# Performance work log

Measured on AMD Instinct MI355X. Metric: run time of the kernel, lower is better.

## Reference

```python
import jax, jax.numpy as jnp
import numpy as np

N_NODES = 100000
N_EDGES = 640000
D_IN = 128
D_OUT = 128
BN_EPS = 1e-5


def setup_inputs() -> dict:
    key = jax.random.key(0)
    k1, k2, k3, k4 = jax.random.split(key, 4)
    x = jax.random.normal(k1, (N_NODES, D_IN), dtype=jnp.float32)
    edge_index = jax.random.randint(k2, (2, N_EDGES), 0, N_NODES, dtype=jnp.int64)
    W = jax.random.normal(k3, (D_IN, D_OUT), dtype=jnp.float32) * (1.0 / np.sqrt(D_IN))
    b = jnp.zeros((D_OUT,), dtype=jnp.float32)
    gamma = jnp.ones((D_OUT,), dtype=jnp.float32)
    beta = jnp.zeros((D_OUT,), dtype=jnp.float32)
    return {"x": x, "edge_index": edge_index, "W": W, "b": b, "gamma": gamma, "beta": beta}


def reference(x, edge_index, W, b, gamma, beta):
    N = x.shape[0]
    # --- GCNConv: add self-loops, symmetric normalization ---
    loop = jnp.arange(N, dtype=edge_index.dtype)
    src = jnp.concatenate([edge_index[0], loop])  # [E+N]
    dst = jnp.concatenate([edge_index[1], loop])  # [E+N]
    deg = jax.ops.segment_sum(jnp.ones_like(dst, dtype=x.dtype), dst, num_segments=N)
    dinv = jax.lax.rsqrt(deg)  # deg >= 1 due to self-loops
    norm = dinv[src] * dinv[dst]  # [E+N]
    # linear transform first (PyG order), then gather-normalize-scatter
    h = x @ W  # [N, D_OUT]
    msg = h[src] * norm[:, None]  # [E+N, D_OUT]
    agg = jax.ops.segment_sum(msg, dst, num_segments=N) + b  # [N, D_OUT]
    # --- ReLU ---
    r = jax.nn.relu(agg)
    # --- BatchNorm over node axis (training-mode batch statistics) ---
    mean = r.mean(axis=0)
    var = r.var(axis=0)
    out = gamma * (r - mean) * jax.lax.rsqrt(var + BN_EPS) + beta
    # dropout: identity in eval/deterministic mode
    return out
```

## Files before the change

### kernel.cpp

```cpp
#include <hip/hip_runtime.h>
#include <hip/hip_bf16.h>

#define N_NODES 100000
#define N_EDGES 640000
#define D 128
#define BN_EPS 1e-5f
#define NB_FILL 2500
#define NB_CVT 6250
#define NREP 64
#define BM 64
#define CS_LD 130
#define SLOTS 16
#define OSLOTS 32

typedef __attribute__((ext_vector_type(8))) short short8;
typedef __attribute__((ext_vector_type(4))) float f32x4;

__device__ inline unsigned int f2bf(float f) {
    unsigned int u = __builtin_bit_cast(unsigned int, f);
    return (u + 0x7FFFu + ((u >> 16) & 1u)) >> 16;
}
__device__ inline float bflo(unsigned int p) { return __builtin_bit_cast(float, p << 16); }
__device__ inline float bfhi(unsigned int p) { return __builtin_bit_cast(float, p & 0xFFFF0000u); }

__global__ void k_zero(int* __restrict__ cnt, float* __restrict__ rep) {
    int i = blockIdx.x * 256 + threadIdx.x;
    if (i < N_NODES) cnt[i] = 0;
    if (i < NREP * 256) rep[i] = 0.0f;
}

__global__ __launch_bounds__(256) void k_prep(const int* __restrict__ ei, int* __restrict__ cnt,
                                              int* __restrict__ buck, int* __restrict__ buck2,
                                              const float* __restrict__ x, uint4* __restrict__ xb,
                                              const float* __restrict__ W,
                                              unsigned short* __restrict__ Wfrag) {
    const int bid = blockIdx.x;
    const int t = threadIdx.x;
    if (bid < NB_CVT) {
        int src = 0, d = 0;
        const bool has_e = (bid < NB_FILL);
        if (has_e) {
            const int e = bid * 256 + t;
            src = ei[e];
            d = ei[N_EDGES + e];
        }
        const size_t i = (size_t)bid * 256 + t;
        const float4* xg = (const float4*)x;
        float4 a = xg[2 * i], c = xg[2 * i + 1];
        int slot = -1;
        if (has_e) slot = atomicAdd(&cnt[d], 1);
        uint4 o;
        o.x = f2bf(a.x) | (f2bf(a.y) << 16);
        o.y = f2bf(a.z) | (f2bf(a.w) << 16);
        o.z = f2bf(c.x) | (f2bf(c.y) << 16);
        o.w = f2bf(c.z) | (f2bf(c.w) << 16);
        xb[i] = o;
        if (has_e) {
            if (slot < SLOTS) buck[(size_t)d * SLOTS + slot] = src;
            else if (slot < SLOTS + OSLOTS) buck2[(size_t)d * OSLOTS + slot - SLOTS] = src;
        }
    } else {
        const int i = (bid - NB_CVT) * 256 + t;
        const int e  = i & 7;
        const int l  = (i >> 3) & 63;
        const int ct = (i >> 9) & 7;
        const int kk = i >> 12;
        const int lr = l & 15, lk = l >> 4;
        const int k   = kk * 32 + lk * 8 + e;
        const int col = ct * 16 + lr;
        Wfrag[i] = (unsigned short)f2bf(W[(size_t)k * D + col]);
    }
}

__global__ __launch_bounds__(1024) void k_gmm(const int* __restrict__ buck,
                                              const int* __restrict__ buck2,
                                              const int* __restrict__ cnt,
                                              const unsigned int* __restrict__ xb,
                                              const unsigned short* __restrict__ Wfrag,
                                              const float* __restrict__ b,
                                              unsigned int* __restrict__ outb,
                                              float* __restrict__ rep) {
    __shared__ __align__(16) char U[BM * CS_LD * 4];
    unsigned int* As_u = (unsigned int*)U;
    float* Cs = (float*)U;
    __shared__ float lsum[16][32];
    __shared__ float lsq[16][32];

    const int t = threadIdx.x;
    const int w = t >> 6;
    const int l = t & 63;
    const int lr = l & 15;
    const int lk = l >> 4;
    const int r0 = blockIdx.x * BM;

    for (int rr = 0; rr < 4; ++rr) {
        const int lrow = w * 4 + rr;
        int n = r0 + lrow; if (n >= N_NODES) n = N_NODES - 1;
        const int deg = cnt[n];
        const float di = rsqrtf((float)(deg + 1));
        const unsigned int hv = xb[(size_t)n * 64 + l];
        const float dd = di * di;
        float ax = bflo(hv) * dd;
        float ay = bfhi(hv) * dd;

        const int m = (deg > SLOTS + OSLOTS) ? (SLOTS + OSLOTS) : deg;
        int s_l = 0; float f_l = 0.0f;
        if (l < m) {
            s_l = (l < SLOTS) ? buck[(size_t)n * SLOTS + l]
                              : buck2[(size_t)n * OSLOTS + l - SLOTS];
            f_l = rsqrtf((float)(cnt[s_l] + 1)) * di;
        }
        for (int k = 0; k < m; k += 8) {
            unsigned int v[8];
            float f[8];
#pragma unroll
            for (int i = 0; i < 8; ++i) {
                const int sj = __builtin_amdgcn_readlane(s_l, k + i);
                f[i] = __builtin_bit_cast(float,
                    __builtin_amdgcn_readlane(__builtin_bit_cast(int, f_l), k + i));
                v[i] = xb[(size_t)sj * 64 + l];
            }
#pragma unroll
            for (int i = 0; i < 8; ++i) {
                ax = fmaf(bflo(v[i]), f[i], ax);
                ay = fmaf(bfhi(v[i]), f[i], ay);
            }
        }
        As_u[lrow * 64 + ((((l >> 2) ^ (lrow & 15)) << 2) | (l & 3))] =
            f2bf(ax) | (f2bf(ay) << 16);
    }
    __syncthreads();

    const int arow = (w & 3) * 16 + lr;
    const uint4* As4 = (const uint4*)U;
    short8 a[4];
#pragma unroll
    for (int kk = 0; kk < 4; ++kk)
        a[kk] = *(const short8*)&As4[arow * 16 + ((kk * 4 + lk) ^ (arow & 15))];
    __syncthreads();

    const int ct0 = (w >> 2) * 2;
    f32x4 acc[2];
    acc[0] = (f32x4)(0.0f);
    acc[1] = (f32x4)(0.0f);
#pragma unroll
    for (int kk = 0; kk < 4; ++kk) {
#pragma unroll
        for (int c = 0; c < 2; ++c) {
            const short8 bb = *(const short8*)(Wfrag + ((((kk * 8 + ct0 + c) << 6) + l) << 3));
            acc[c] = __builtin_amdgcn_mfma_f32_16x16x32_bf16(a[kk], bb, acc[c], 0, 0, 0);
        }
    }

    float s[2] = {0.0f, 0.0f}, s2[2] = {0.0f, 0.0f};
#pragma unroll
    for (int c = 0; c < 2; ++c) {
        const int ct = ct0 + c;
        const float bias = b[ct * 16 + lr];
#pragma unroll
        for (int r = 0; r < 4; ++r) {
            const int lrow = (w & 3) * 16 + lk * 4 + r;
            const float v = fmaxf(acc[c][r] + bias, 0.0f);
            if (r0 + lrow < N_NODES) {
                s[c] += v;
                s2[c] = fmaf(v, v, s2[c]);
            }
            Cs[lrow * CS_LD + ct * 16 + lr] = v;
        }
    }
#pragma unroll
    for (int c = 0; c < 2; ++c) {
        s[c]  += __shfl_xor(s[c], 16);  s[c]  += __shfl_xor(s[c], 32);
        s2[c] += __shfl_xor(s2[c], 16); s2[c] += __shfl_xor(s2[c], 32);
    }
    if (l < 16) {
#pragma unroll
        for (int c = 0; c < 2; ++c) {
            lsum[w][c * 16 + lr] = s[c];
            lsq[w][c * 16 + lr]  = s2[c];
        }
    }
    __syncthreads();

#pragma unroll
    for (int i = 0; i < 1; ++i) { }
#pragma unroll
    for (int i = 0; i < 1; ++i) {
        const int v0 = t;
#pragma unroll
        for (int p = 0; p < 1; ++p) { }
    }
    {
        const int v = t;
        const int row = v >> 4;
        const int q   = v & 15;
        if (r0 + row < N_NODES) {
            const float* p = &Cs[row * CS_LD + q * 8];
            uint4 o;
            o.x = f2bf(p[0]) | (f2bf(p[1]) << 16);
            o.y = f2bf(p[2]) | (f2bf(p[3]) << 16);
            o.z = f2bf(p[4]) | (f2bf(p[5]) << 16);
            o.w = f2bf(p[6]) | (f2bf(p[7]) << 16);
            ((uint4*)outb)[(size_t)(r0 + row) * 16 + q] = o;
        }
    }

    if (t < 128) {
        const int g = t >> 5;
        const int cc = t & 31;
        const float ssum = lsum[4 * g + 0][cc] + lsum[4 * g + 1][cc]
                         + lsum[4 * g + 2][cc] + lsum[4 * g + 3][cc];
        const float ssq  = lsq[4 * g + 0][cc] + lsq[4 * g + 1][cc]
                         + lsq[4 * g + 2][cc] + lsq[4 * g + 3][cc];
        const int col = g * 32 + cc;
        float* r = rep + (blockIdx.x & (NREP - 1)) * 256;
        atomicAdd(&r[col],       ssum);
        atomicAdd(&r[128 + col], ssq);
    }
}

__global__ __launch_bounds__(256) void k_red(const float* __restrict__ rep,
                                             const float* __restrict__ gamma,
                                             const float* __restrict__ beta,
                                             float* __restrict__ sclsft) {
    __shared__ float sh[256];
    const int t = threadIdx.x;
    float s = 0.0f;
    for (int r = 0; r < NREP; ++r) s += rep[r * 256 + t];
    sh[t] = s;
    __syncthreads();
    if (t < 128) {
        const float inv_n = 1.0f / (float)N_NODES;
        const float mean = sh[t] * inv_n;
        const float var = sh[128 + t] * inv_n - mean * mean;
        const float sc = gamma[t] * rsqrtf(var + BN_EPS);
        sclsft[t]       = sc;
        sclsft[128 + t] = beta[t] - mean * sc;
    }
}

__global__ __launch_bounds__(256) void k_norm(const uint4* __restrict__ outb,
                                              float4* __restrict__ out,
                                              const float* __restrict__ sclsft) {
    __shared__ float sc[256];
    const int t = threadIdx.x;
    sc[t] = sclsft[t];
    __syncthreads();
    const int i = blockIdx.x * 256 + t;
    if (i >= N_NODES * 16) return;
    const int c0 = (i & 15) * 8;
    const uint4 v = outb[i];
    float4 o0, o1;
    o0.x = fmaf(bflo(v.x), sc[c0 + 0], sc[128 + c0 + 0]);
    o0.y = fmaf(bfhi(v.x), sc[c0 + 1], sc[128 + c0 + 1]);
    o0.z = fmaf(bflo(v.y), sc[c0 + 2], sc[128 + c0 + 2]);
    o0.w = fmaf(bfhi(v.y), sc[c0 + 3], sc[128 + c0 + 3]);
    o1.x = fmaf(bflo(v.z), sc[c0 + 4], sc[128 + c0 + 4]);
    o1.y = fmaf(bfhi(v.z), sc[c0 + 5], sc[128 + c0 + 5]);
    o1.z = fmaf(bflo(v.w), sc[c0 + 6], sc[128 + c0 + 6]);
    o1.w = fmaf(bfhi(v.w), sc[c0 + 7], sc[128 + c0 + 7]);
    out[(size_t)i * 2]     = o0;
    out[(size_t)i * 2 + 1] = o1;
}

extern "C" void kernel_launch(void* const* d_in, const int* in_sizes, int n_in,
                              void* d_out, int out_size, void* d_ws, size_t ws_size,
                              hipStream_t stream) {
    const float* x     = (const float*)d_in[0];
    const int*   ei    = (const int*)d_in[1];
    const float* W     = (const float*)d_in[2];
    const float* b     = (const float*)d_in[3];
    const float* gamma = (const float*)d_in[4];
    const float* beta  = (const float*)d_in[5];
    float* out = (float*)d_out;

    char* ws = (char*)d_ws;
    int*            cnt    = (int*)(ws + 0);
    float*          rep    = (float*)(ws + (512u << 10));
    float*          sclsft = (float*)(ws + (640u << 10));
    unsigned short* Wfrag  = (unsigned short*)(ws + (704u << 10));
    int*            buck   = (int*)(ws + (1024u << 10));
    int*            buck2  = (int*)(ws + (8192u << 10));
    unsigned int*   xb     = (unsigned int*)(ws + (24576u << 10));
    unsigned int*   outb   = (unsigned int*)(ws + (57344u << 10));

    k_zero<<<(N_NODES + 255) / 256, 256, 0, stream>>>(cnt, rep);
    k_prep<<<NB_CVT + 64, 256, 0, stream>>>(ei, cnt, buck, buck2, x, (uint4*)xb, W, Wfrag);
    k_gmm<<<(N_NODES + BM - 1) / BM, 1024, 0, stream>>>(buck, buck2, cnt, xb, Wfrag, b,
                                                        outb, rep);
    k_red<<<1, 256, 0, stream>>>(rep, gamma, beta, sclsft);
    k_norm<<<(N_NODES * 16 + 255) / 256, 256, 0, stream>>>((const uint4*)outb, (float4*)out,
                                                           sclsft);
}
```

Measured before the change: 120.0 us.

## Partition edge bucketing per XCD to cut cross-die atomic contention

Edge bucketing moves into 313 dedicated blocks, each handling 8 edges per thread. Counters and 8-slot buckets are replicated per XCD (indexed by blockIdx&7), so the atomics stay local to one die, and a shared overflow list catches the rest. A new k_dinv kernel sums the per-XCD counts into dinv and a packed prefix word that k_gmm uses to locate neighbour indices. k_zero is replaced by hipMemsetAsync. The change adds a launch, more metadata traffic, a scattered 8x bucket layout and prefix decoding in the gather loop, and it assumes blockIdx&7 matches the XCD placement.

Measured after the change: 127.5 us. +6.3%, slower.

```diff
diff --git a/kernel.cpp b/kernel.cpp
--- a/kernel.cpp
+++ b/kernel.cpp
@@ -5,13 +5,13 @@
 #define N_EDGES 640000
 #define D 128
 #define BN_EPS 1e-5f
-#define NB_FILL 2500
+#define NB_FILLB 313
 #define NB_CVT 6250
 #define NREP 64
 #define BM 64
 #define CS_LD 130
-#define SLOTS 16
-#define OSLOTS 32
+#define XSLOTS 8
+#define OSLOTS 24
 
 typedef __attribute__((ext_vector_type(8))) short short8;
 typedef __attribute__((ext_vector_type(4))) float f32x4;
@@ -23,44 +23,43 @@
 __device__ inline float bflo(unsigned int p) { return __builtin_bit_cast(float, p << 16); }
 __device__ inline float bfhi(unsigned int p) { return __builtin_bit_cast(float, p & 0xFFFF0000u); }
 
-__global__ void k_zero(int* __restrict__ cnt, float* __restrict__ rep) {
-    int i = blockIdx.x * 256 + threadIdx.x;
-    if (i < N_NODES) cnt[i] = 0;
-    if (i < NREP * 256) rep[i] = 0.0f;
-}
-
-__global__ __launch_bounds__(256) void k_prep(const int* __restrict__ ei, int* __restrict__ cnt,
-                                              int* __restrict__ buck, int* __restrict__ buck2,
+__global__ __launch_bounds__(256) void k_prep(const int* __restrict__ ei, int* __restrict__ cnt8,
+                                              int* __restrict__ ocnt,
+                                              int* __restrict__ buck8, int* __restrict__ buck2,
                                               const float* __restrict__ x, uint4* __restrict__ xb,
                                               const float* __restrict__ W,
                                               unsigned short* __restrict__ Wfrag) {
     const int bid = blockIdx.x;
     const int t = threadIdx.x;
-    if (bid < NB_CVT) {
-        int src = 0, d = 0;
-        const bool has_e = (bid < NB_FILL);
-        if (has_e) {
-            const int e = bid * 256 + t;
-            src = ei[e];
-            d = ei[N_EDGES + e];
-        }
-        const size_t i = (size_t)bid * 256 + t;
+    if (bid < NB_FILLB) {
+        const int xcd = bid & 7;
+#pragma unroll
+        for (int it = 0; it < 8; ++it) {
+            const int e = (it * NB_FILLB + bid) * 256 + t;
+            if (e < N_EDGES) {
+                const int src = ei[e];
+                const int d = ei[N_EDGES + e];
+                const int slot = atomicAdd(&cnt8[xcd * N_NODES + d], 1);
+                if (slot < XSLOTS)
+                    buck8[(((size_t)xcd * N_NODES + d) << 3) + slot] = src;
+                else {
+                    const int o = atomicAdd(&ocnt[d], 1);
+                    if (o < OSLOTS) buck2[(size_t)d * OSLOTS + o] = src;
+                }
+            }
+        }
+    } else if (bid < NB_FILLB + NB_CVT) {
+        const size_t i = (size_t)(bid - NB_FILLB) * 256 + t;
         const float4* xg = (const float4*)x;
         float4 a = xg[2 * i], c = xg[2 * i + 1];
-        int slot = -1;
-        if (has_e) slot = atomicAdd(&cnt[d], 1);
         uint4 o;
         o.x = f2bf(a.x) | (f2bf(a.y) << 16);
         o.y = f2bf(a.z) | (f2bf(a.w) << 16);
         o.z = f2bf(c.x) | (f2bf(c.y) << 16);
         o.w = f2bf(c.z) | (f2bf(c.w) << 16);
         xb[i] = o;
-        if (has_e) {
-            if (slot < SLOTS) buck[(size_t)d * SLOTS + slot] = src;
-            else if (slot < SLOTS + OSLOTS) buck2[(size_t)d * OSLOTS + slot - SLOTS] = src;
-        }
     } else {
-        const int i = (bid - NB_CVT) * 256 + t;
+        const int i = (bid - NB_FILLB - NB_CVT) * 256 + t;
         const int e  = i & 7;
         const int l  = (i >> 3) & 63;
         const int ct = (i >> 9) & 7;
@@ -72,9 +71,31 @@
     }
 }
 
-__global__ __launch_bounds__(1024) void k_gmm(const int* __restrict__ buck,
+__global__ __launch_bounds__(256) void k_dinv(const int* __restrict__ cnt8,
+                                              const int* __restrict__ ocnt,
+                                              float* __restrict__ dinv,
+                                              uint2* __restrict__ pfxovf) {
+    const int n = blockIdx.x * 256 + threadIdx.x;
+    if (n >= N_NODES) return;
+    int deg = 0, pre = 0;
+    unsigned long long v = 0;
+#pragma unroll
+    for (int k = 0; k < 8; ++k) {
+        const int c = cnt8[k * N_NODES + n];
+        deg += c;
+        pre += (c > XSLOTS) ? XSLOTS : c;
+        v |= ((unsigned long long)pre) << (7 * k);
+    }
+    int ov = ocnt[n]; if (ov > OSLOTS) ov = OSLOTS;
+    v |= ((unsigned long long)ov) << 56;
+    dinv[n] = rsqrtf((float)(deg + 1));
+    pfxovf[n] = make_uint2((unsigned)(v & 0xffffffffu), (unsigned)(v >> 32));
+}
+
+__global__ __launch_bounds__(1024) void k_gmm(const int* __restrict__ buck8,
                                               const int* __restrict__ buck2,
-                                              const int* __restrict__ cnt,
+                                              const float* __restrict__ dinv,
+                                              const uint2* __restrict__ pfxovf,
                                               const unsigned int* __restrict__ xb,
                                               const unsigned short* __restrict__ Wfrag,
                                               const float* __restrict__ b,
@@ -96,19 +117,35 @@
     for (int rr = 0; rr < 4; ++rr) {
         const int lrow = w * 4 + rr;
         int n = r0 + lrow; if (n >= N_NODES) n = N_NODES - 1;
-        const int deg = cnt[n];
-        const float di = rsqrtf((float)(deg + 1));
+        const float di = dinv[n];
+        const uint2 pf = pfxovf[n];
+        const unsigned long long v64 = ((unsigned long long)pf.y << 32) | pf.x;
+        int P[8];
+#pragma unroll
+        for (int j = 0; j < 8; ++j) P[j] = (int)((v64 >> (7 * j)) & 127u);
+        const int ov = (int)((v64 >> 56) & 31u);
+        const int m_in = P[7];
+        int m = m_in + ov; if (m > 64) m = 64;
+
         const unsigned int hv = xb[(size_t)n * 64 + l];
         const float dd = di * di;
         float ax = bflo(hv) * dd;
         float ay = bfhi(hv) * dd;
 
-        const int m = (deg > SLOTS + OSLOTS) ? (SLOTS + OSLOTS) : deg;
         int s_l = 0; float f_l = 0.0f;
         if (l < m) {
-            s_l = (l < SLOTS) ? buck[(size_t)n * SLOTS + l]
-                              : buck2[(size_t)n * OSLOTS + l - SLOTS];
-            f_l = rsqrtf((float)(cnt[s_l] + 1)) * di;
+            int s;
+            if (l < m_in) {
+                int k = 0, base = 0;
+#pragma unroll
+                for (int j = 0; j < 7; ++j)
+                    if (l >= P[j]) { k = j + 1; base = P[j]; }
+                s = buck8[(((size_t)k * N_NODES + n) << 3) + (l - base)];
+            } else {
+                s = buck2[(size_t)n * OSLOTS + (l - m_in)];
+            }
+            s_l = s;
+            f_l = dinv[s] * di;
         }
         for (int k = 0; k < m; k += 8) {
             unsigned int v[8];
@@ -182,18 +219,10 @@
     }
     __syncthreads();
 
-#pragma unroll
-    for (int i = 0; i < 1; ++i) { }
-#pragma unroll
-    for (int i = 0; i < 1; ++i) {
-        const int v0 = t;
-#pragma unroll
-        for (int p = 0; p < 1; ++p) { }
-    }
     {
-        const int v = t;
-        const int row = v >> 4;
-        const int q   = v & 15;
+        const int vv = t;
+        const int row = vv >> 4;
+        const int q   = vv & 15;
         if (r0 + row < N_NODES) {
             const float* p = &Cs[row * CS_LD + q * 8];
             uint4 o;
@@ -275,19 +304,24 @@
     float* out = (float*)d_out;
 
     char* ws = (char*)d_ws;
-    int*            cnt    = (int*)(ws + 0);
-    float*          rep    = (float*)(ws + (512u << 10));
-    float*          sclsft = (float*)(ws + (640u << 10));
-    unsigned short* Wfrag  = (unsigned short*)(ws + (704u << 10));
-    int*            buck   = (int*)(ws + (1024u << 10));
-    int*            buck2  = (int*)(ws + (8192u << 10));
-    unsigned int*   xb     = (unsigned int*)(ws + (24576u << 10));
-    unsigned int*   outb   = (unsigned int*)(ws + (57344u << 10));
-
-    k_zero<<<(N_NODES + 255) / 256, 256, 0, stream>>>(cnt, rep);
-    k_prep<<<NB_CVT + 64, 256, 0, stream>>>(ei, cnt, buck, buck2, x, (uint4*)xb, W, Wfrag);
-    k_gmm<<<(N_NODES + BM - 1) / BM, 1024, 0, stream>>>(buck, buck2, cnt, xb, Wfrag, b,
-                                                        outb, rep);
+    int*            cnt8   = (int*)(ws + 0);
+    int*            ocnt   = (int*)(ws + 3200000);
+    float*          rep    = (float*)(ws + 3600000);
+    float*          sclsft = (float*)(ws + 3670016);
+    unsigned short* Wfrag  = (unsigned short*)(ws + 3680000);
+    float*          dinv   = (float*)(ws + 3720000);
+    uint2*          pfxovf = (uint2*)(ws + 4120000);
+    int*            buck2  = (int*)(ws + 4920000);
+    int*            buck8  = (int*)(ws + 14520000);
+    unsigned int*   xb     = (unsigned int*)(ws + 40120000);
+    unsigned int*   outb   = (unsigned int*)(ws + 65720000);
+
+    hipMemsetAsync(ws, 0, 3665536, stream);
+    k_prep<<<NB_FILLB + NB_CVT + 64, 256, 0, stream>>>(ei, cnt8, ocnt, buck8, buck2,
+                                                       x, (uint4*)xb, W, Wfrag);
+    k_dinv<<<(N_NODES + 255) / 256, 256, 0, stream>>>(cnt8, ocnt, dinv, pfxovf);
+    k_gmm<<<(N_NODES + BM - 1) / BM, 1024, 0, stream>>>(buck8, buck2, dinv, pfxovf, xb,
+                                                        Wfrag, b, outb, rep);
     k_red<<<1, 256, 0, stream>>>(rep, gamma, beta, sclsft);
     k_norm<<<(N_NODES * 16 + 255) / 256, 256, 0, stream>>>((const uint4*)outb, (float4*)out,
                                                            sclsft);
```
